# Performance work log

Hardware: AMD Instinct MI355X
Metric: run time of the kernel (lower is better)

## Reference

```python
import jax, jax.numpy as jnp
import numpy as np

B, LQ, LK, D = 8, 2048, 2048, 128
NEG = -100000.0


def setup_inputs() -> dict:
    key = jax.random.key(0)
    kq, kk, kv, km = jax.random.split(key, 4)
    q = jax.random.normal(kq, (B, LQ, D), dtype=jnp.float32)
    k = jax.random.normal(kk, (B, LK, D), dtype=jnp.float32)
    v = jax.random.normal(kv, (B, LK, D), dtype=jnp.float32)
    mask = jax.random.randint(km, (B, LQ, LK), 0, 2, dtype=jnp.int32)
    return {"q": q, "k": k, "v": v, "mask": mask}


def reference(q, k, v, mask):
    # atten_score = q @ k^T / sqrt(d)   [B, Lq, Lk]
    scores = jnp.einsum("bqd,bkd->bqk", q, k) / jnp.sqrt(jnp.float32(q.shape[-1]))
    # mask_mod == 2: additive mask, masked positions pushed to large negative
    scores = scores + mask.astype(jnp.float32) * NEG
    # sigmoid instead of softmax (no normalization across keys)
    attn = jax.nn.sigmoid(scores)
    return jnp.einsum("bqk,bkd->bqd", attn, v)
```

## Files before the change

### kernel.cpp

```cpp
#include <hip/hip_runtime.h>
#include <hip/hip_bf16.h>

#define B_   8
#define LQ_  2048
#define LK_  2048
#define D_   128
#define QBLK 64
#define KBLK 64
#define NT   (LK_ / KBLK)
#define THREADS 512
#define SCALE 0.08838834764831845f

typedef __attribute__((ext_vector_type(8))) __bf16 bf16x8;
typedef __attribute__((ext_vector_type(4))) __bf16 bf16x4;
typedef __attribute__((ext_vector_type(4))) float  f32x4;
typedef __attribute__((ext_vector_type(4))) float  fx4;

#define QS_OFF 0
#define KS_OFF 8704
#define VT_OFF 17408
#define PS_OFF 26624
#define SMEM_ELEMS 31744

__global__ __launch_bounds__(THREADS, 2)
void sigattn_kernel(const float* __restrict__ q, const float* __restrict__ k,
                    const float* __restrict__ v, const int* __restrict__ mask,
                    float* __restrict__ out)
{
    __shared__ __bf16 smem[SMEM_ELEMS];

    const int tid  = threadIdx.x;
    const int lane = tid & 63;
    const int wid  = tid >> 6;
    const int qg   = wid & 3;
    const int kg   = wid >> 2;
    const int l15  = lane & 15;
    const int g    = lane >> 4;

    const int bid   = blockIdx.x;
    const int b     = bid & 7;
    const int q0    = (bid >> 3) * QBLK;

    const float* qb = q + (size_t)b * LQ_ * D_ + (size_t)q0 * D_;
    const float* kb = k + (size_t)b * LK_ * D_;
    const float* vb = v + (size_t)b * LK_ * D_;
    const int*   mb = mask + (size_t)b * LQ_ * LK_ + (size_t)q0 * LK_;
    float*       ob = out + (size_t)b * LQ_ * D_ + (size_t)q0 * D_;

    __bf16* Qs = smem + QS_OFF;
    __bf16* Ks = smem + KS_OFF;
    __bf16* Vt = smem + VT_OFF;
    __bf16* Ps = smem + PS_OFF + wid * 640;

    const int dv  = tid & 127;
    const int kq8 = tid >> 7;

    int mcur[8];

#pragma unroll
    for (int i = 0; i < 4; ++i) {
        int idx = tid + i * THREADS;
        int row = idx >> 5, c4 = idx & 31;
        fx4 f = *(const fx4*)(qb + row * D_ + c4 * 4);
        bf16x4 w; w[0]=(__bf16)f[0]; w[1]=(__bf16)f[1]; w[2]=(__bf16)f[2]; w[3]=(__bf16)f[3];
        *(bf16x4*)(Qs + row * 136 + c4 * 4) = w;
    }
#pragma unroll
    for (int i = 0; i < 4; ++i) {
        int idx = tid + i * THREADS;
        int row = idx >> 5, c4 = idx & 31;
        fx4 f = *(const fx4*)(kb + row * D_ + c4 * 4);
        bf16x4 w; w[0]=(__bf16)f[0]; w[1]=(__bf16)f[1]; w[2]=(__bf16)f[2]; w[3]=(__bf16)f[3];
        *(bf16x4*)(Ks + row * 136 + c4 * 4) = w;
    }
#pragma unroll
    for (int i = 0; i < 4; ++i) {
        int quad = kq8 + i * 4;
        bf16x4 w;
#pragma unroll
        for (int j = 0; j < 4; ++j) w[j] = (__bf16)vb[(quad * 4 + j) * D_ + dv];
        *(bf16x4*)(Vt + dv * 72 + quad * 4) = w;
    }
#pragma unroll
    for (int n2 = 0; n2 < 2; ++n2)
#pragma unroll
        for (int r = 0; r < 4; ++r)
            mcur[n2 * 4 + r] = mb[(qg * 16 + 4 * g + r) * LK_ + (kg * 32 + n2 * 16 + l15)];

    __syncthreads();

    bf16x8 qfrag[4];
#pragma unroll
    for (int dblk = 0; dblk < 4; ++dblk)
        qfrag[dblk] = *(const bf16x8*)(Qs + (qg * 16 + l15) * 136 + dblk * 32 + g * 8);

    f32x4 oacc[8];
#pragma unroll
    for (int nb = 0; nb < 8; ++nb) oacc[nb] = (f32x4){0.f, 0.f, 0.f, 0.f};

    for (int t = 0; t < NT; ++t) {
        const bool more = (t + 1 < NT);

        fx4   kreg[4];
        float vreg[16];
        int   mnxt[8];
        if (more) {
            const int kt = (t + 1) * KBLK;
#pragma unroll
            for (int i = 0; i < 4; ++i) {
                int idx = tid + i * THREADS;
                int row = idx >> 5, c4 = idx & 31;
                kreg[i] = *(const fx4*)(kb + (kt + row) * D_ + c4 * 4);
            }
#pragma unroll
            for (int i = 0; i < 4; ++i) {
                int quad = kq8 + i * 4;
#pragma unroll
                for (int j = 0; j < 4; ++j)
                    vreg[i * 4 + j] = vb[(kt + quad * 4 + j) * D_ + dv];
            }
#pragma unroll
            for (int n2 = 0; n2 < 2; ++n2)
#pragma unroll
                for (int r = 0; r < 4; ++r)
                    mnxt[n2 * 4 + r] = mb[(qg * 16 + 4 * g + r) * LK_ + (kt + kg * 32 + n2 * 16 + l15)];
        }

        f32x4 sacc[2];
        sacc[0] = (f32x4){0.f, 0.f, 0.f, 0.f};
        sacc[1] = (f32x4){0.f, 0.f, 0.f, 0.f};
#pragma unroll
        for (int n2 = 0; n2 < 2; ++n2) {
            const __bf16* krow = Ks + (kg * 32 + n2 * 16 + l15) * 136 + g * 8;
#pragma unroll
            for (int dblk = 0; dblk < 4; ++dblk) {
                bf16x8 bfr = *(const bf16x8*)(krow + dblk * 32);
                sacc[n2] = __builtin_amdgcn_mfma_f32_16x16x32_bf16(qfrag[dblk], bfr, sacc[n2], 0, 0, 0);
            }
        }

#pragma unroll
        for (int n2 = 0; n2 < 2; ++n2)
#pragma unroll
            for (int r = 0; r < 4; ++r) {
                float s = sacc[n2][r] * SCALE;
                float p = (mcur[n2 * 4 + r] != 0) ? 0.0f : 1.0f / (1.0f + __expf(-s));
                Ps[(4 * g + r) * 40 + n2 * 16 + l15] = (__bf16)p;
            }

        bf16x8 pfrag = *(const bf16x8*)(Ps + l15 * 40 + g * 8);
#pragma unroll
        for (int nb = 0; nb < 8; ++nb) {
            bf16x8 vfr = *(const bf16x8*)(Vt + (nb * 16 + l15) * 72 + kg * 32 + g * 8);
            oacc[nb] = __builtin_amdgcn_mfma_f32_16x16x32_bf16(pfrag, vfr, oacc[nb], 0, 0, 0);
        }

        __syncthreads();

        if (more) {
#pragma unroll
            for (int i = 0; i < 4; ++i) {
                int idx = tid + i * THREADS;
                int row = idx >> 5, c4 = idx & 31;
                bf16x4 w;
                w[0]=(__bf16)kreg[i][0]; w[1]=(__bf16)kreg[i][1];
                w[2]=(__bf16)kreg[i][2]; w[3]=(__bf16)kreg[i][3];
                *(bf16x4*)(Ks + row * 136 + c4 * 4) = w;
            }
#pragma unroll
            for (int i = 0; i < 4; ++i) {
                int quad = kq8 + i * 4;
                bf16x4 w;
#pragma unroll
                for (int j = 0; j < 4; ++j) w[j] = (__bf16)vreg[i * 4 + j];
                *(bf16x4*)(Vt + dv * 72 + quad * 4) = w;
            }
#pragma unroll
            for (int j = 0; j < 8; ++j) mcur[j] = mnxt[j];
        }

        __syncthreads();
    }

    float* red = (float*)smem;
    if (kg == 0) {
#pragma unroll
        for (int nb = 0; nb < 8; ++nb)
#pragma unroll
            for (int r = 0; r < 4; ++r)
                red[(qg * 16 + 4 * g + r) * 132 + nb * 16 + l15] = oacc[nb][r];
    }
    __syncthreads();
    if (kg == 1) {
#pragma unroll
        for (int nb = 0; nb < 8; ++nb)
#pragma unroll
            for (int r = 0; r < 4; ++r) {
                int row = qg * 16 + 4 * g + r;
                float val = red[row * 132 + nb * 16 + l15] + oacc[nb][r];
                ob[(size_t)row * D_ + nb * 16 + l15] = val;
            }
    }
}

extern "C" void kernel_launch(void* const* d_in, const int* in_sizes, int n_in,
                              void* d_out, int out_size, void* d_ws, size_t ws_size,
                              hipStream_t stream) {
    const float* q    = (const float*)d_in[0];
    const float* k    = (const float*)d_in[1];
    const float* v    = (const float*)d_in[2];
    const int*   mask = (const int*)d_in[3];
    float*       out  = (float*)d_out;

    dim3 grid(B_ * (LQ_ / QBLK));
    dim3 block(THREADS);
    sigattn_kernel<<<grid, block, 0, stream>>>(q, k, v, mask, out);
}
```

Measured before the change: 237.6 us.

## Split key range across two blocks with atomic reduction and swizzled LDS

Splits the key dimension into two halves handled by separate blocks. This doubles the grid so more CUs and waves are busy, and partial outputs are combined with atomicAdd into a buffer zeroed by hipMemsetAsync. The Q tile now loads straight into registers instead of going through LDS, the K and V tiles use XOR-swizzled unpadded LDS layouts, the reciprocal uses the hardware rcp intrinsic, and launch bounds target 4 blocks per CU. In exchange it adds an extra memset launch, float atomics that make the summation order nondeterministic, and a dependence on out_size being an element count.

```diff
diff --git a/kernel.cpp b/kernel.cpp
--- a/kernel.cpp
+++ b/kernel.cpp
@@ -7,7 +7,9 @@
 #define D_   128
 #define QBLK 64
 #define KBLK 64
-#define NT   (LK_ / KBLK)
+#define KSPLIT 2
+#define KRANGE (LK_ / KSPLIT)
+#define NT    (KRANGE / KBLK)
 #define THREADS 512
 #define SCALE 0.08838834764831845f
 
@@ -16,13 +18,12 @@
 typedef __attribute__((ext_vector_type(4))) float  f32x4;
 typedef __attribute__((ext_vector_type(4))) float  fx4;
 
-#define QS_OFF 0
-#define KS_OFF 8704
-#define VT_OFF 17408
-#define PS_OFF 26624
-#define SMEM_ELEMS 31744
-
-__global__ __launch_bounds__(THREADS, 2)
+#define KS_OFF 0
+#define VT_OFF 8192
+#define PS_OFF 16384
+#define SMEM_ELEMS 21504
+
+__global__ __launch_bounds__(THREADS, 4)
 void sigattn_kernel(const float* __restrict__ q, const float* __restrict__ k,
                     const float* __restrict__ v, const int* __restrict__ mask,
                     float* __restrict__ out)
@@ -37,33 +38,40 @@
     const int l15  = lane & 15;
     const int g    = lane >> 4;
 
-    const int bid   = blockIdx.x;
-    const int b     = bid & 7;
-    const int q0    = (bid >> 3) * QBLK;
+    const int bid  = blockIdx.x;
+    const int b    = bid & 7;
+    const int rest = bid >> 3;
+    const int q0   = (rest >> 1) * QBLK;
+    const int ks   = rest & 1;
 
     const float* qb = q + (size_t)b * LQ_ * D_ + (size_t)q0 * D_;
-    const float* kb = k + (size_t)b * LK_ * D_;
-    const float* vb = v + (size_t)b * LK_ * D_;
-    const int*   mb = mask + (size_t)b * LQ_ * LK_ + (size_t)q0 * LK_;
+    const float* kb = k + (size_t)b * LK_ * D_ + (size_t)ks * KRANGE * D_;
+    const float* vb = v + (size_t)b * LK_ * D_ + (size_t)ks * KRANGE * D_;
+    const int*   mb = mask + (size_t)b * LQ_ * LK_ + (size_t)q0 * LK_ + (size_t)ks * KRANGE;
     float*       ob = out + (size_t)b * LQ_ * D_ + (size_t)q0 * D_;
 
-    __bf16* Qs = smem + QS_OFF;
     __bf16* Ks = smem + KS_OFF;
     __bf16* Vt = smem + VT_OFF;
     __bf16* Ps = smem + PS_OFF + wid * 640;
 
     const int dv  = tid & 127;
     const int kq8 = tid >> 7;
+    const int vswz = ((dv & 7) << 3);
 
     int mcur[8];
 
-#pragma unroll
-    for (int i = 0; i < 4; ++i) {
-        int idx = tid + i * THREADS;
-        int row = idx >> 5, c4 = idx & 31;
-        fx4 f = *(const fx4*)(qb + row * D_ + c4 * 4);
-        bf16x4 w; w[0]=(__bf16)f[0]; w[1]=(__bf16)f[1]; w[2]=(__bf16)f[2]; w[3]=(__bf16)f[3];
-        *(bf16x4*)(Qs + row * 136 + c4 * 4) = w;
+    bf16x8 qfrag[4];
+    {
+        const float* qrow = qb + (qg * 16 + l15) * D_;
+#pragma unroll
+        for (int dblk = 0; dblk < 4; ++dblk) {
+            fx4 f0 = *(const fx4*)(qrow + dblk * 32 + g * 8);
+            fx4 f1 = *(const fx4*)(qrow + dblk * 32 + g * 8 + 4);
+            bf16x8 w;
+#pragma unroll
+            for (int j = 0; j < 4; ++j) { w[j] = (__bf16)f0[j]; w[4 + j] = (__bf16)f1[j]; }
+            qfrag[dblk] = w;
+        }
     }
 #pragma unroll
     for (int i = 0; i < 4; ++i) {
@@ -71,7 +79,7 @@
         int row = idx >> 5, c4 = idx & 31;
         fx4 f = *(const fx4*)(kb + row * D_ + c4 * 4);
         bf16x4 w; w[0]=(__bf16)f[0]; w[1]=(__bf16)f[1]; w[2]=(__bf16)f[2]; w[3]=(__bf16)f[3];
-        *(bf16x4*)(Ks + row * 136 + c4 * 4) = w;
+        *(bf16x4*)(Ks + row * 128 + ((c4 * 4) ^ ((row & 7) << 3))) = w;
     }
 #pragma unroll
     for (int i = 0; i < 4; ++i) {
@@ -79,7 +87,7 @@
         bf16x4 w;
 #pragma unroll
         for (int j = 0; j < 4; ++j) w[j] = (__bf16)vb[(quad * 4 + j) * D_ + dv];
-        *(bf16x4*)(Vt + dv * 72 + quad * 4) = w;
+        *(bf16x4*)(Vt + dv * 64 + ((quad * 4) ^ vswz)) = w;
     }
 #pragma unroll
     for (int n2 = 0; n2 < 2; ++n2)
@@ -87,16 +95,11 @@
         for (int r = 0; r < 4; ++r)
             mcur[n2 * 4 + r] = mb[(qg * 16 + 4 * g + r) * LK_ + (kg * 32 + n2 * 16 + l15)];
 
+    f32x4 oacc[8];
+#pragma unroll
+    for (int nb = 0; nb < 8; ++nb) oacc[nb] = (f32x4){0.f, 0.f, 0.f, 0.f};
+
     __syncthreads();
-
-    bf16x8 qfrag[4];
-#pragma unroll
-    for (int dblk = 0; dblk < 4; ++dblk)
-        qfrag[dblk] = *(const bf16x8*)(Qs + (qg * 16 + l15) * 136 + dblk * 32 + g * 8);
-
-    f32x4 oacc[8];
-#pragma unroll
-    for (int nb = 0; nb < 8; ++nb) oacc[nb] = (f32x4){0.f, 0.f, 0.f, 0.f};
 
     for (int t = 0; t < NT; ++t) {
         const bool more = (t + 1 < NT);
@@ -131,10 +134,12 @@
         sacc[1] = (f32x4){0.f, 0.f, 0.f, 0.f};
 #pragma unroll
         for (int n2 = 0; n2 < 2; ++n2) {
-            const __bf16* krow = Ks + (kg * 32 + n2 * 16 + l15) * 136 + g * 8;
+            const int krow = kg * 32 + n2 * 16 + l15;
+            const __bf16* kbase = Ks + krow * 128;
+            const int kswz = (krow & 7) << 3;
 #pragma unroll
             for (int dblk = 0; dblk < 4; ++dblk) {
-                bf16x8 bfr = *(const bf16x8*)(krow + dblk * 32);
+                bf16x8 bfr = *(const bf16x8*)(kbase + ((dblk * 32 + g * 8) ^ kswz));
                 sacc[n2] = __builtin_amdgcn_mfma_f32_16x16x32_bf16(qfrag[dblk], bfr, sacc[n2], 0, 0, 0);
             }
         }
@@ -144,14 +149,17 @@
 #pragma unroll
             for (int r = 0; r < 4; ++r) {
                 float s = sacc[n2][r] * SCALE;
-                float p = (mcur[n2 * 4 + r] != 0) ? 0.0f : 1.0f / (1.0f + __expf(-s));
+                float p = (mcur[n2 * 4 + r] != 0)
+                            ? 0.0f
+                            : __builtin_amdgcn_rcpf(1.0f + __expf(-s));
                 Ps[(4 * g + r) * 40 + n2 * 16 + l15] = (__bf16)p;
             }
 
         bf16x8 pfrag = *(const bf16x8*)(Ps + l15 * 40 + g * 8);
 #pragma unroll
         for (int nb = 0; nb < 8; ++nb) {
-            bf16x8 vfr = *(const bf16x8*)(Vt + (nb * 16 + l15) * 72 + kg * 32 + g * 8);
+            const int vrow = nb * 16 + l15;
+            bf16x8 vfr = *(const bf16x8*)(Vt + vrow * 64 + ((kg * 32 + g * 8) ^ ((vrow & 7) << 3)));
             oacc[nb] = __builtin_amdgcn_mfma_f32_16x16x32_bf16(pfrag, vfr, oacc[nb], 0, 0, 0);
         }
 
@@ -165,7 +173,7 @@
                 bf16x4 w;
                 w[0]=(__bf16)kreg[i][0]; w[1]=(__bf16)kreg[i][1];
                 w[2]=(__bf16)kreg[i][2]; w[3]=(__bf16)kreg[i][3];
-                *(bf16x4*)(Ks + row * 136 + c4 * 4) = w;
+                *(bf16x4*)(Ks + row * 128 + ((c4 * 4) ^ ((row & 7) << 3))) = w;
             }
 #pragma unroll
             for (int i = 0; i < 4; ++i) {
@@ -173,7 +181,7 @@
                 bf16x4 w;
 #pragma unroll
                 for (int j = 0; j < 4; ++j) w[j] = (__bf16)vreg[i * 4 + j];
-                *(bf16x4*)(Vt + dv * 72 + quad * 4) = w;
+                *(bf16x4*)(Vt + dv * 64 + ((quad * 4) ^ vswz)) = w;
             }
 #pragma unroll
             for (int j = 0; j < 8; ++j) mcur[j] = mnxt[j];
@@ -188,7 +196,7 @@
         for (int nb = 0; nb < 8; ++nb)
 #pragma unroll
             for (int r = 0; r < 4; ++r)
-                red[(qg * 16 + 4 * g + r) * 132 + nb * 16 + l15] = oacc[nb][r];
+                red[(qg * 16 + 4 * g + r) * 128 + nb * 16 + l15] = oacc[nb][r];
     }
     __syncthreads();
     if (kg == 1) {
@@ -197,8 +205,8 @@
 #pragma unroll
             for (int r = 0; r < 4; ++r) {
                 int row = qg * 16 + 4 * g + r;
-                float val = red[row * 132 + nb * 16 + l15] + oacc[nb][r];
-                ob[(size_t)row * D_ + nb * 16 + l15] = val;
+                float val = red[row * 128 + nb * 16 + l15] + oacc[nb][r];
+                atomicAdd(&ob[(size_t)row * D_ + nb * 16 + l15], val);
             }
     }
 }
@@ -212,7 +220,9 @@
     const int*   mask = (const int*)d_in[3];
     float*       out  = (float*)d_out;
 
-    dim3 grid(B_ * (LQ_ / QBLK));
+    hipMemsetAsync(out, 0, (size_t)out_size * sizeof(float), stream);
+
+    dim3 grid(B_ * (LQ_ / QBLK) * KSPLIT);
     dim3 block(THREADS);
     sigattn_kernel<<<grid, block, 0, stream>>>(q, k, v, mask, out);
 }
```

New measurement: 283.0 us. 1.19x slower.
